# Kernel optimization log

Measured on AMD Instinct MI355X. Metric: run time of the kernel, lower is better.

## Reference

```python
import jax, jax.numpy as jnp
import numpy as np
from functools import partial

N_NODES = 50000
N_EDGES = 600000
IN_C = 128
HID = 128
OUT_C = 8
N_GRAPHS = 64
EPS = 1e-5


def setup_inputs() -> dict:
    key = jax.random.key(0)
    ks = jax.random.split(key, 16)
    inp = {
        "x": jax.random.normal(ks[0], (N_NODES, IN_C), dtype=jnp.float32),
        "edge_index": jax.random.randint(ks[1], (2, N_EDGES), 0, N_NODES, dtype=jnp.int64),
        "batch": jnp.sort(jax.random.randint(ks[2], (N_NODES,), 0, N_GRAPHS, dtype=jnp.int64)),
    }
    dims = [(IN_C, HID), (HID, HID), (HID, HID)]
    for i, (din, dout) in enumerate(dims):
        inp[f"W{i}"] = jax.random.normal(ks[3 + i], (din, dout), dtype=jnp.float32) / np.sqrt(din)
        inp[f"b{i}"] = jnp.zeros((dout,), dtype=jnp.float32)
        inp[f"g{i}"] = jnp.ones((dout,), dtype=jnp.float32)
        inp[f"be{i}"] = jnp.zeros((dout,), dtype=jnp.float32)
    inp["Wh"] = jax.random.normal(ks[10], (HID, OUT_C), dtype=jnp.float32) / np.sqrt(HID)
    inp["bh"] = jnp.zeros((OUT_C,), dtype=jnp.float32)
    return inp


def gcn_conv(x, W, b, src, dst, dinv_src, dinv_dst):
    # transform then normalized scatter-add aggregation (add_self_loops=False)
    h = x @ W  # [N, D]
    msg = (dinv_src * dinv_dst)[:, None] * h[src]  # [E, D]
    out = jax.ops.segment_sum(msg, dst, num_segments=N_NODES)
    return out + b


def batchnorm(x, g, be):
    mu = jnp.mean(x, axis=0)
    var = jnp.mean((x - mu) ** 2, axis=0)  # biased, as torch BN training
    return (x - mu) * jax.lax.rsqrt(var + EPS) * g + be


def reference(x, edge_index, batch, W0, b0, g0, be0, W1, b1, g1, be1, W2, b2, g2, be2, Wh, bh):
    src, dst = edge_index[0], edge_index[1]
    deg = jax.ops.segment_sum(jnp.ones((N_EDGES,), x.dtype), dst, num_segments=N_NODES)
    dinv = jnp.where(deg > 0, jax.lax.rsqrt(jnp.maximum(deg, 1.0)), 0.0)
    dinv_src, dinv_dst = dinv[src], dinv[dst]

    for W, b, g, be in [(W0, b0, g0, be0), (W1, b1, g1, be1), (W2, b2, g2, be2)]:
        x = gcn_conv(x, W, b, src, dst, dinv_src, dinv_dst)
        x = jax.nn.relu(batchnorm(x, g, be))  # dropout is identity in eval

    # global mean pool over graphs
    sums = jax.ops.segment_sum(x, batch, num_segments=N_GRAPHS)
    cnts = jax.ops.segment_sum(jnp.ones((N_NODES,), x.dtype), batch, num_segments=N_GRAPHS)
    pooled = sums / jnp.maximum(cnts, 1.0)[:, None]
    return pooled @ Wh + bh
```

## Files before the change

### kernel.cpp

```cpp
#include <hip/hip_runtime.h>
#include <hip/hip_fp16.h>

#define NODES 50000
#define EDGES 600000
#define C     128
#define NGRAPH 64
#define EPSBN 1e-5f
#define BUCKET 64
#define AGGNB 6250
#define POOLROWS 32
#define POOLB ((NODES + POOLROWS - 1) / POOLROWS)

typedef short v8s __attribute__((ext_vector_type(8)));
typedef float v4f __attribute__((ext_vector_type(4)));

#define OFF_DEGCNT 0u
#define OFF_CURSOR 200192u
#define OFF_STATS  400384u
#define OFF_PSUM   424960u
#define ZERO_BYTES 457728u
#define OFF_DINV   457728u
#define OFF_BPACK  657920u
#define OFF_EC     756224u
#define OFF_BUFH   13556224u
#define OFF_BUFA   26356224u

static __device__ __forceinline__ unsigned short f2bf(float f) {
    unsigned u = __float_as_uint(f);
    u += 0x7fffu + ((u >> 16) & 1u);
    return (unsigned short)(u >> 16);
}
static __device__ __forceinline__ float bflo(unsigned u) { return __uint_as_float(u << 16); }
static __device__ __forceinline__ float bfhi(unsigned u) { return __uint_as_float(u & 0xffff0000u); }
static __device__ __forceinline__ float bf1(unsigned short s) { return __uint_as_float(((unsigned)s) << 16); }

static __device__ __forceinline__ void gld_lds16(const void* g, void* l) {
    __builtin_amdgcn_global_load_lds(
        (const __attribute__((address_space(1))) void*)g,
        (__attribute__((address_space(3))) void*)l, 16, 0, 0);
}

__global__ void deg_kernel(const int* __restrict__ dst, int* __restrict__ degcnt) {
    int e4 = blockIdx.x * 256 + threadIdx.x;
    if (e4 < EDGES / 4) {
        int4 d = *(const int4*)&dst[e4 * 4];
        atomicAdd(&degcnt[d.x], 1);
        atomicAdd(&degcnt[d.y], 1);
        atomicAdd(&degcnt[d.z], 1);
        atomicAdd(&degcnt[d.w], 1);
    }
}

__global__ __launch_bounds__(256) void dinvpack_kernel(const int* __restrict__ degcnt,
                                                       float* __restrict__ dinv,
                                                       const float* __restrict__ W0,
                                                       const float* __restrict__ W1,
                                                       const float* __restrict__ W2,
                                                       short* __restrict__ Bp) {
    int bid = blockIdx.x, t = threadIdx.x;
    if (bid < 196) {
        int i = bid * 256 + t;
        if (i < NODES) {
            int v = degcnt[i];
            dinv[i] = (v > 0) ? rsqrtf((float)v) : 0.f;
        }
        return;
    }
    int id = (bid - 196) * 256 + t;
    int l = id >> 11;
    int f = id & 2047;
    const float* W = (l == 0) ? W0 : (l == 1) ? W1 : W2;
    int lane = f & 63, nbks = f >> 6;
    int nb = nbks >> 2, ks = nbks & 3;
    int q = lane >> 4, n = lane & 15;
    v8s o;
    #pragma unroll
    for (int j = 0; j < 8; j++)
        o[j] = (short)f2bf(W[(ks * 32 + q * 8 + j) * 128 + nb * 16 + n]);
    *(v8s*)&Bp[id * 8] = o;
}

__global__ void fill_kernel(const int* __restrict__ src, const int* __restrict__ dst,
                            int* __restrict__ cursor, const float* __restrict__ dinv,
                            unsigned* __restrict__ ec) {
    int e2 = blockIdx.x * 256 + threadIdx.x;
    if (e2 < EDGES / 2) {
        int2 s = *(const int2*)&src[e2 * 2];
        int2 d = *(const int2*)&dst[e2 * 2];
        float w0 = dinv[s.x] * dinv[d.x];
        float w1 = dinv[s.y] * dinv[d.y];
        unsigned r0 = (unsigned)s.x | ((unsigned)__half_as_ushort(__float2half(w0)) << 16);
        unsigned r1 = (unsigned)s.y | ((unsigned)__half_as_ushort(__float2half(w1)) << 16);
        int p0 = atomicAdd(&cursor[d.x], 1);
        if (p0 < BUCKET) ec[d.x * BUCKET + p0] = r0;
        int p1 = atomicAdd(&cursor[d.y], 1);
        if (p1 < BUCKET) ec[d.y * BUCKET + p1] = r1;
    }
}

template<bool A32>
__global__ __launch_bounds__(256) void gemm_kernel(
    const void* __restrict__ Ain, const short* __restrict__ Bpg,
    unsigned short* __restrict__ Hout, const float* __restrict__ stats,
    const float* __restrict__ g, const float* __restrict__ be) {
    __shared__ short Apk[8320];
    __shared__ short Bpk[16384];
    __shared__ float sbn[256];
    int t = threadIdx.x;
    int r0 = blockIdx.x * 64;
    if (stats) {
        if (t < 128) {
            float s = 0.f, sq = 0.f;
            #pragma unroll
            for (int r = 0; r < 8; r++) {
                s  += stats[r * 256 + t];
                sq += stats[r * 256 + 128 + t];
            }
            float mean = s * (1.0f / NODES);
            float var = sq * (1.0f / NODES) - mean * mean;
            float sc = g[t] * rsqrtf(var + EPSBN);
            sbn[t] = sc;
            sbn[128 + t] = be[t] - mean * sc;
        }
        __syncthreads();
    }
    {
        int wl = t & 63;
        int wb = t & 192;
        #pragma unroll
        for (int i = 0; i < 8; i++) {
            int cb = i * 256 + wb;
            gld_lds16(&Bpg[(size_t)(cb + wl) * 8], &Bpk[cb * 8]);
        }
    }
    #pragma unroll
    for (int i = 0; i < 4; i++) {
        int f = t + 256 * i;
        int row = f >> 4, kf = f & 15;
        int gr = r0 + row;
        float v[8];
        #pragma unroll
        for (int e = 0; e < 8; e++) v[e] = 0.f;
        if (gr < NODES) {
            if (A32) {
                const float* Ap = (const float*)Ain + (size_t)gr * C + kf * 8;
                float4 lo = *(const float4*)Ap;
                float4 hi = *(const float4*)(Ap + 4);
                v[0]=lo.x; v[1]=lo.y; v[2]=lo.z; v[3]=lo.w;
                v[4]=hi.x; v[5]=hi.y; v[6]=hi.z; v[7]=hi.w;
            } else {
                const unsigned short* Ap = (const unsigned short*)Ain + (size_t)gr * C + kf * 8;
                uint4 raw = *(const uint4*)Ap;
                v[0]=bflo(raw.x); v[1]=bfhi(raw.x); v[2]=bflo(raw.y); v[3]=bfhi(raw.y);
                v[4]=bflo(raw.z); v[5]=bfhi(raw.z); v[6]=bflo(raw.w); v[7]=bfhi(raw.w);
            }
        }
        if (stats) {
            #pragma unroll
            for (int e = 0; e < 8; e++) {
                int c = kf * 8 + e;
                v[e] = fmaxf(0.f, fmaf(v[e], sbn[c], sbn[128 + c]));
            }
        }
        v8s af;
        #pragma unroll
        for (int e = 0; e < 8; e++) af[e] = (short)f2bf(v[e]);
        int mb = row >> 4, m = row & 15, ks = kf >> 2, q = kf & 3;
        *(v8s*)&Apk[(mb * 4 + ks) * 520 + (q * 16 + m) * 8] = af;
    }
    __syncthreads();
    int lane = t & 63, mb = t >> 6;
    v4f acc[8];
    #pragma unroll
    for (int nb = 0; nb < 8; nb++) acc[nb] = 0.f;
    #pragma unroll
    for (int ks = 0; ks < 4; ks++) {
        v8s aF = *(const v8s*)&Apk[(mb * 4 + ks) * 520 + lane * 8];
        #pragma unroll
        for (int nb = 0; nb < 8; nb++) {
            v8s bF = *(const v8s*)&Bpk[((nb * 4 + ks) * 64 + lane) * 8];
            acc[nb] = __builtin_amdgcn_mfma_f32_16x16x32_bf16(aF, bF, acc[nb], 0, 0, 0);
        }
    }
    int q = lane >> 4, n = lane & 15;
    #pragma unroll
    for (int nb = 0; nb < 8; nb++) {
        #pragma unroll
        for (int r = 0; r < 4; r++)
            Apk[mb * 2080 + (q * 4 + r) * 128 + nb * 16 + n] = (short)f2bf(acc[nb][r]);
    }
    #pragma unroll
    for (int i = 0; i < 4; i++) {
        int idx = lane + 64 * i;
        int row = idx >> 4, colv = (idx & 15) * 8;
        int gr = r0 + mb * 16 + row;
        if (gr < NODES)
            *(uint4*)&Hout[(size_t)gr * C + colv] = *(const uint4*)&Apk[mb * 2080 + row * 128 + colv];
    }
}

__global__ __launch_bounds__(512) void agg_kernel(
    const unsigned short* __restrict__ H, const int* __restrict__ deg,
    const unsigned* __restrict__ ec, unsigned short* __restrict__ Aout,
    float* __restrict__ stats) {
    int t = threadIdx.x;
    int lane = t & 63;
    int half = lane >> 5;
    int sl = lane & 31;
    int wid = (blockIdx.x * 512 + t) >> 6;
    float a0 = 0.f, a1 = 0.f, a2 = 0.f, a3 = 0.f;
    unsigned o0 = 0, o1 = 0;
    if (wid < NODES) {
        int beg = wid * BUCKET;
        int end = beg + min(deg[wid], BUCKET);
        int i = beg;
        for (; i + 16 <= end; i += 16) {
            unsigned e[8];
            #pragma unroll
            for (int u = 0; u < 8; u++) e[u] = ec[i + 2 * u + half];
            uint2 v[8];
            #pragma unroll
            for (int u = 0; u < 8; u++)
                v[u] = *(const uint2*)&H[(size_t)(e[u] & 0xffffu) * C + sl * 4];
            #pragma unroll
            for (int u = 0; u < 8; u++) {
                float w = __half2float(__ushort_as_half((unsigned short)(e[u] >> 16)));
                a0 = fmaf(w, bflo(v[u].x), a0);
                a1 = fmaf(w, bfhi(v[u].x), a1);
                a2 = fmaf(w, bflo(v[u].y), a2);
                a3 = fmaf(w, bfhi(v[u].y), a3);
            }
        }
        if (i < end) {
            int last = end - 1;
            unsigned e[8];
            #pragma unroll
            for (int u = 0; u < 8; u++) {
                int idx = i + 2 * u + half;
                unsigned r = ec[idx < end ? idx : last];
                e[u] = (idx < end) ? r : (r & 0xffffu);
            }
            uint2 v[8];
            #pragma unroll
            for (int u = 0; u < 8; u++)
                v[u] = *(const uint2*)&H[(size_t)(e[u] & 0xffffu) * C + sl * 4];
            #pragma unroll
            for (int u = 0; u < 8; u++) {
                float w = __half2float(__ushort_as_half((unsigned short)(e[u] >> 16)));
                a0 = fmaf(w, bflo(v[u].x), a0);
                a1 = fmaf(w, bfhi(v[u].x), a1);
                a2 = fmaf(w, bflo(v[u].y), a2);
                a3 = fmaf(w, bfhi(v[u].y), a3);
            }
        }
        a0 += __shfl_xor(a0, 32);
        a1 += __shfl_xor(a1, 32);
        a2 += __shfl_xor(a2, 32);
        a3 += __shfl_xor(a3, 32);
        o0 = ((unsigned)f2bf(a1) << 16) | (unsigned)f2bf(a0);
        o1 = ((unsigned)f2bf(a3) << 16) | (unsigned)f2bf(a2);
        if (half == 0)
            *(uint2*)&Aout[(size_t)wid * C + sl * 4] = make_uint2(o0, o1);
    }
    __shared__ float red[2048];
    int w = t >> 6;
    {
        float r0v = bflo(o0), r1v = bfhi(o0), r2v = bflo(o1), r3v = bfhi(o1);
        float* dst = &red[1024 * half + w * 128 + sl * 4];
        if (half) { r0v *= r0v; r1v *= r1v; r2v *= r2v; r3v *= r3v; }
        dst[0] = r0v; dst[1] = r1v; dst[2] = r2v; dst[3] = r3v;
    }
    __syncthreads();
    float* sr = stats + (blockIdx.x & 7) * 256;
    if (t < 128) {
        float vs = 0.f, vq = 0.f;
        #pragma unroll
        for (int k = 0; k < 8; k++) {
            vs += red[k * 128 + t];
            vq += red[1024 + k * 128 + t];
        }
        atomicAdd(&sr[t], vs);
        atomicAdd(&sr[128 + t], vq);
    }
}

__global__ __launch_bounds__(256) void pool_kernel(const unsigned short* __restrict__ X,
                                                   const int* __restrict__ batch,
                                                   const float* __restrict__ stats,
                                                   const float* __restrict__ g,
                                                   const float* __restrict__ be,
                                                   float* __restrict__ psum) {
    int t = threadIdx.x;
    __shared__ float sbn[256];
    if (t < 128) {
        float s = 0.f, sq = 0.f;
        #pragma unroll
        for (int r = 0; r < 8; r++) {
            s  += stats[r * 256 + t];
            sq += stats[r * 256 + 128 + t];
        }
        float mean = s * (1.0f / NODES);
        float var = sq * (1.0f / NODES) - mean * mean;
        float scv = g[t] * rsqrtf(var + EPSBN);
        sbn[t] = scv;
        sbn[128 + t] = be[t] - mean * scv;
    }
    __syncthreads();
    int lane = t & 63, w = t >> 6;
    int c0 = lane * 2;
    int r0 = blockIdx.x * POOLROWS + w * 8;
    float* pr = psum + (blockIdx.x & 3) * (NGRAPH * C);
    if (r0 >= NODES) return;
    int nr = min(8, NODES - r0);
    float sc0 = sbn[c0], sh0 = sbn[128 + c0];
    float sc1 = sbn[c0 + 1], sh1 = sbn[128 + c0 + 1];
    unsigned uv[8]; int gb[8];
    #pragma unroll
    for (int j = 0; j < 8; j++) {
        int r = r0 + ((j < nr) ? j : (nr - 1));
        uv[j] = *(const unsigned*)&X[(size_t)r * C + c0];
        gb[j] = batch[r];
    }
    float ax = 0.f, ay = 0.f;
    int cur = gb[0];
    #pragma unroll
    for (int j = 0; j < 8; j++) {
        if (gb[j] != cur) {
            atomicAdd(&pr[cur * C + c0], ax);
            atomicAdd(&pr[cur * C + c0 + 1], ay);
            ax = 0.f; ay = 0.f; cur = gb[j];
        }
        float m = (j < nr) ? 1.f : 0.f;
        ax += m * fmaxf(0.f, fmaf(bflo(uv[j]), sc0, sh0));
        ay += m * fmaxf(0.f, fmaf(bfhi(uv[j]), sc1, sh1));
    }
    atomicAdd(&pr[cur * C + c0], ax);
    atomicAdd(&pr[cur * C + c0 + 1], ay);
}

__global__ __launch_bounds__(128) void head_kernel(const float* __restrict__ psum,
                                                   const int* __restrict__ batch,
                                                   const float* __restrict__ Wh,
                                                   const float* __restrict__ bh,
                                                   float* __restrict__ out) {
    int g = blockIdx.x, ch = threadIdx.x;
    __shared__ int sb[2];
    if (ch < 2) {
        int tgt = g + ch;
        int lo = 0, hi = NODES;
        while (lo < hi) { int m = (lo + hi) >> 1; if (batch[m] < tgt) lo = m + 1; else hi = m; }
        sb[ch] = lo;
    }
    float pv = 0.f;
    #pragma unroll
    for (int rep = 0; rep < 4; rep++) pv += psum[rep * (NGRAPH * C) + g * C + ch];
    __shared__ float red[128 * 8];
    #pragma unroll
    for (int o = 0; o < 8; o++) red[ch * 8 + o] = pv * Wh[ch * 8 + o];
    __syncthreads();
    for (int off = 64; off >= 1; off >>= 1) {
        if (ch < off) {
            #pragma unroll
            for (int o = 0; o < 8; o++) red[ch * 8 + o] += red[(ch + off) * 8 + o];
        }
        __syncthreads();
    }
    if (ch < 8) {
        float inv = 1.0f / fmaxf((float)(sb[1] - sb[0]), 1.0f);
        out[g * 8 + ch] = fmaf(red[ch], inv, bh[ch]);
    }
}

extern "C" void kernel_launch(void* const* d_in, const int* in_sizes, int n_in,
                              void* d_out, int out_size, void* d_ws, size_t ws_size,
                              hipStream_t stream) {
    (void)in_sizes; (void)n_in; (void)out_size; (void)ws_size;
    const float* x    = (const float*)d_in[0];
    const int*   ei   = (const int*)d_in[1];
    const int*   batch= (const int*)d_in[2];
    const float* W0   = (const float*)d_in[3];
    const float* g0   = (const float*)d_in[5];
    const float* be0  = (const float*)d_in[6];
    const float* W1   = (const float*)d_in[7];
    const float* g1   = (const float*)d_in[9];
    const float* be1  = (const float*)d_in[10];
    const float* W2   = (const float*)d_in[11];
    const float* g2   = (const float*)d_in[13];
    const float* be2  = (const float*)d_in[14];
    const float* Wh   = (const float*)d_in[15];
    const float* bh   = (const float*)d_in[16];
    float* out = (float*)d_out;

    char* ws = (char*)d_ws;
    int*   degcnt = (int*)(ws + OFF_DEGCNT);
    int*   cursor = (int*)(ws + OFF_CURSOR);
    float* stats  = (float*)(ws + OFF_STATS);
    float* psum   = (float*)(ws + OFF_PSUM);
    float* dinv   = (float*)(ws + OFF_DINV);
    short* bpack  = (short*)(ws + OFF_BPACK);
    unsigned* ec  = (unsigned*)(ws + OFF_EC);
    unsigned short* bufH = (unsigned short*)(ws + OFF_BUFH);
    unsigned short* bufA = (unsigned short*)(ws + OFF_BUFA);

    (void)hipMemsetAsync(ws, 0, ZERO_BYTES, stream);

    deg_kernel<<<(EDGES / 4 + 255) / 256, 256, 0, stream>>>(ei + EDGES, degcnt);
    dinvpack_kernel<<<196 + 24, 256, 0, stream>>>(degcnt, dinv, W0, W1, W2, bpack);
    fill_kernel<<<(EDGES / 2 + 255) / 256, 256, 0, stream>>>(ei, ei + EDGES, cursor, dinv, ec);

    const int GB = (NODES + 63) / 64;

    gemm_kernel<true><<<GB, 256, 0, stream>>>(x, bpack, bufH, nullptr, nullptr, nullptr);
    agg_kernel<<<AGGNB, 512, 0, stream>>>(bufH, degcnt, ec, bufA, stats + 0);
    gemm_kernel<false><<<GB, 256, 0, stream>>>(bufA, bpack + 16384, bufH, stats + 0, g0, be0);
    agg_kernel<<<AGGNB, 512, 0, stream>>>(bufH, degcnt, ec, bufA, stats + 2048);
    gemm_kernel<false><<<GB, 256, 0, stream>>>(bufA, bpack + 32768, bufH, stats + 2048, g1, be1);
    agg_kernel<<<AGGNB, 512, 0, stream>>>(bufH, degcnt, ec, bufA, stats + 4096);
    pool_kernel<<<POOLB, 256, 0, stream>>>(bufA, batch, stats + 4096, g2, be2, psum);
    head_kernel<<<NGRAPH, 128, 0, stream>>>(psum, batch, Wh, bh, out);
}
```

Measured before the change: 302.8 us.

## Merge degree count into fill, store 16-bit edge sources, split aggregation by channel halves

Removes the separate degree kernel by reusing the fill cursor as the degree count. Edge buckets now store only the 16-bit source index, and the normalization weight is recomputed in the aggregation kernel from dinv. Each aggregation block now covers one half of the channels, so the 64-channel halves of a node are processed by different blocks and block order is interleaved to share cache. This halves the edge-list footprint and drops one preprocessing pass. In exchange it adds a dinv gather per edge, doubles the edge-list reads across channel halves, and relies on node ids fitting in 16 bits.

Measured after the change: 304.9 us. No clear change (+0.7%).

```diff
diff --git a/kernel.cpp b/kernel.cpp
--- a/kernel.cpp
+++ b/kernel.cpp
@@ -7,23 +7,22 @@
 #define NGRAPH 64
 #define EPSBN 1e-5f
 #define BUCKET 64
-#define AGGNB 6250
+#define AGGNB 12504
 #define POOLROWS 32
 #define POOLB ((NODES + POOLROWS - 1) / POOLROWS)
 
 typedef short v8s __attribute__((ext_vector_type(8)));
 typedef float v4f __attribute__((ext_vector_type(4)));
 
-#define OFF_DEGCNT 0u
-#define OFF_CURSOR 200192u
-#define OFF_STATS  400384u
-#define OFF_PSUM   424960u
-#define ZERO_BYTES 457728u
-#define OFF_DINV   457728u
-#define OFF_BPACK  657920u
-#define OFF_EC     756224u
-#define OFF_BUFH   13556224u
-#define OFF_BUFA   26356224u
+#define OFF_CURSOR 0u
+#define OFF_STATS  200192u
+#define OFF_PSUM   224768u
+#define ZERO_BYTES 257536u
+#define OFF_DINV   257536u
+#define OFF_BPACK  457728u
+#define OFF_EC     556032u
+#define OFF_BUFH   6956032u
+#define OFF_BUFA   19756032u
 
 static __device__ __forceinline__ unsigned short f2bf(float f) {
     unsigned u = __float_as_uint(f);
@@ -40,14 +39,16 @@
         (__attribute__((address_space(3))) void*)l, 16, 0, 0);
 }
 
-__global__ void deg_kernel(const int* __restrict__ dst, int* __restrict__ degcnt) {
-    int e4 = blockIdx.x * 256 + threadIdx.x;
-    if (e4 < EDGES / 4) {
-        int4 d = *(const int4*)&dst[e4 * 4];
-        atomicAdd(&degcnt[d.x], 1);
-        atomicAdd(&degcnt[d.y], 1);
-        atomicAdd(&degcnt[d.z], 1);
-        atomicAdd(&degcnt[d.w], 1);
+__global__ void fill_kernel(const int* __restrict__ src, const int* __restrict__ dst,
+                            int* __restrict__ cursor, unsigned short* __restrict__ ec16) {
+    int e2 = blockIdx.x * 256 + threadIdx.x;
+    if (e2 < EDGES / 2) {
+        int2 s = *(const int2*)&src[e2 * 2];
+        int2 d = *(const int2*)&dst[e2 * 2];
+        int p0 = atomicAdd(&cursor[d.x], 1);
+        if (p0 < BUCKET) ec16[d.x * BUCKET + p0] = (unsigned short)s.x;
+        int p1 = atomicAdd(&cursor[d.y], 1);
+        if (p1 < BUCKET) ec16[d.y * BUCKET + p1] = (unsigned short)s.y;
     }
 }
 
@@ -78,24 +79,6 @@
     for (int j = 0; j < 8; j++)
         o[j] = (short)f2bf(W[(ks * 32 + q * 8 + j) * 128 + nb * 16 + n]);
     *(v8s*)&Bp[id * 8] = o;
-}
-
-__global__ void fill_kernel(const int* __restrict__ src, const int* __restrict__ dst,
-                            int* __restrict__ cursor, const float* __restrict__ dinv,
-                            unsigned* __restrict__ ec) {
-    int e2 = blockIdx.x * 256 + threadIdx.x;
-    if (e2 < EDGES / 2) {
-        int2 s = *(const int2*)&src[e2 * 2];
-        int2 d = *(const int2*)&dst[e2 * 2];
-        float w0 = dinv[s.x] * dinv[d.x];
-        float w1 = dinv[s.y] * dinv[d.y];
-        unsigned r0 = (unsigned)s.x | ((unsigned)__half_as_ushort(__float2half(w0)) << 16);
-        unsigned r1 = (unsigned)s.y | ((unsigned)__half_as_ushort(__float2half(w1)) << 16);
-        int p0 = atomicAdd(&cursor[d.x], 1);
-        if (p0 < BUCKET) ec[d.x * BUCKET + p0] = r0;
-        int p1 = atomicAdd(&cursor[d.y], 1);
-        if (p1 < BUCKET) ec[d.y * BUCKET + p1] = r1;
-    }
 }
 
 template<bool A32>
@@ -201,86 +184,96 @@
 
 __global__ __launch_bounds__(512) void agg_kernel(
     const unsigned short* __restrict__ H, const int* __restrict__ deg,
-    const unsigned* __restrict__ ec, unsigned short* __restrict__ Aout,
-    float* __restrict__ stats) {
+    const float* __restrict__ dinv, const unsigned short* __restrict__ ec16,
+    unsigned short* __restrict__ Aout, float* __restrict__ stats) {
     int t = threadIdx.x;
     int lane = t & 63;
     int half = lane >> 5;
     int sl = lane & 31;
-    int wid = (blockIdx.x * 512 + t) >> 6;
-    float a0 = 0.f, a1 = 0.f, a2 = 0.f, a3 = 0.f;
-    unsigned o0 = 0, o1 = 0;
+    int b = blockIdx.x;
+    int xs = b & 7;
+    int h = xs >> 2;
+    int o = (b >> 3) * 4 + (xs & 3);
+    int w = t >> 6;
+    int wid = o * 8 + w;
+    int h64 = h * 64;
+    float a0 = 0.f, a1 = 0.f;
+    unsigned o0 = 0;
     if (wid < NODES) {
-        int beg = wid * BUCKET;
-        int end = beg + min(deg[wid], BUCKET);
+        int dg = min(deg[wid], BUCKET);
+        float dd = dinv[wid];
+        int beg = wid * BUCKET, end = beg + dg;
+        const unsigned short* Hc = H + h64 + sl * 2;
         int i = beg;
         for (; i + 16 <= end; i += 16) {
-            unsigned e[8];
-            #pragma unroll
-            for (int u = 0; u < 8; u++) e[u] = ec[i + 2 * u + half];
-            uint2 v[8];
-            #pragma unroll
-            for (int u = 0; u < 8; u++)
-                v[u] = *(const uint2*)&H[(size_t)(e[u] & 0xffffu) * C + sl * 4];
+            uint4 ra = *(const uint4*)&ec16[i];
+            uint4 rb = *(const uint4*)&ec16[i + 8];
+            unsigned wd[8] = {ra.x, ra.y, ra.z, ra.w, rb.x, rb.y, rb.z, rb.w};
+            int rec[8];
+            #pragma unroll
+            for (int u = 0; u < 8; u++) rec[u] = (wd[u] >> (16 * half)) & 0xffff;
+            float dv[8];
+            #pragma unroll
+            for (int u = 0; u < 8; u++) dv[u] = dinv[rec[u]];
+            unsigned v[8];
+            #pragma unroll
+            for (int u = 0; u < 8; u++) v[u] = *(const unsigned*)&Hc[(size_t)rec[u] * C];
             #pragma unroll
             for (int u = 0; u < 8; u++) {
-                float w = __half2float(__ushort_as_half((unsigned short)(e[u] >> 16)));
-                a0 = fmaf(w, bflo(v[u].x), a0);
-                a1 = fmaf(w, bfhi(v[u].x), a1);
-                a2 = fmaf(w, bflo(v[u].y), a2);
-                a3 = fmaf(w, bfhi(v[u].y), a3);
+                float wt = dv[u] * dd;
+                a0 = fmaf(wt, bflo(v[u]), a0);
+                a1 = fmaf(wt, bfhi(v[u]), a1);
             }
         }
         if (i < end) {
-            int last = end - 1;
-            unsigned e[8];
+            int rl = ec16[end - 1];
+            uint4 ra = *(const uint4*)&ec16[i];
+            uint4 rb = *(const uint4*)&ec16[i + 8];
+            unsigned wd[8] = {ra.x, ra.y, ra.z, ra.w, rb.x, rb.y, rb.z, rb.w};
+            int rec[8]; float ms[8];
             #pragma unroll
             for (int u = 0; u < 8; u++) {
                 int idx = i + 2 * u + half;
-                unsigned r = ec[idx < end ? idx : last];
-                e[u] = (idx < end) ? r : (r & 0xffffu);
-            }
-            uint2 v[8];
-            #pragma unroll
-            for (int u = 0; u < 8; u++)
-                v[u] = *(const uint2*)&H[(size_t)(e[u] & 0xffffu) * C + sl * 4];
+                int r = (wd[u] >> (16 * half)) & 0xffff;
+                bool valid = idx < end;
+                rec[u] = valid ? r : rl;
+                ms[u] = valid ? 1.f : 0.f;
+            }
+            float dv[8];
+            #pragma unroll
+            for (int u = 0; u < 8; u++) dv[u] = dinv[rec[u]];
+            unsigned v[8];
+            #pragma unroll
+            for (int u = 0; u < 8; u++) v[u] = *(const unsigned*)&Hc[(size_t)rec[u] * C];
             #pragma unroll
             for (int u = 0; u < 8; u++) {
-                float w = __half2float(__ushort_as_half((unsigned short)(e[u] >> 16)));
-                a0 = fmaf(w, bflo(v[u].x), a0);
-                a1 = fmaf(w, bfhi(v[u].x), a1);
-                a2 = fmaf(w, bflo(v[u].y), a2);
-                a3 = fmaf(w, bfhi(v[u].y), a3);
+                float wt = ms[u] * dv[u] * dd;
+                a0 = fmaf(wt, bflo(v[u]), a0);
+                a1 = fmaf(wt, bfhi(v[u]), a1);
             }
         }
         a0 += __shfl_xor(a0, 32);
         a1 += __shfl_xor(a1, 32);
-        a2 += __shfl_xor(a2, 32);
-        a3 += __shfl_xor(a3, 32);
         o0 = ((unsigned)f2bf(a1) << 16) | (unsigned)f2bf(a0);
-        o1 = ((unsigned)f2bf(a3) << 16) | (unsigned)f2bf(a2);
         if (half == 0)
-            *(uint2*)&Aout[(size_t)wid * C + sl * 4] = make_uint2(o0, o1);
-    }
-    __shared__ float red[2048];
-    int w = t >> 6;
+            *(unsigned*)&Aout[(size_t)wid * C + h64 + sl * 2] = o0;
+    }
+    __shared__ float red[1024];
     {
-        float r0v = bflo(o0), r1v = bfhi(o0), r2v = bflo(o1), r3v = bfhi(o1);
-        float* dst = &red[1024 * half + w * 128 + sl * 4];
-        if (half) { r0v *= r0v; r1v *= r1v; r2v *= r2v; r3v *= r3v; }
-        dst[0] = r0v; dst[1] = r1v; dst[2] = r2v; dst[3] = r3v;
+        float rx = bflo(o0), ry = bfhi(o0);
+        if (half) { rx *= rx; ry *= ry; }
+        red[half * 512 + w * 64 + sl * 2]     = rx;
+        red[half * 512 + w * 64 + sl * 2 + 1] = ry;
     }
     __syncthreads();
-    float* sr = stats + (blockIdx.x & 7) * 256;
+    float* sr = stats + ((b >> 3) & 7) * 256;
     if (t < 128) {
-        float vs = 0.f, vq = 0.f;
-        #pragma unroll
-        for (int k = 0; k < 8; k++) {
-            vs += red[k * 128 + t];
-            vq += red[1024 + k * 128 + t];
-        }
-        atomicAdd(&sr[t], vs);
-        atomicAdd(&sr[128 + t], vq);
+        int role = t >> 6;
+        int c = t & 63;
+        float vv = 0.f;
+        #pragma unroll
+        for (int k = 0; k < 8; k++) vv += red[role * 512 + k * 64 + c];
+        atomicAdd(&sr[role * 128 + h64 + c], vv);
     }
 }
 
@@ -392,30 +385,28 @@
     float* out = (float*)d_out;
 
     char* ws = (char*)d_ws;
-    int*   degcnt = (int*)(ws + OFF_DEGCNT);
     int*   cursor = (int*)(ws + OFF_CURSOR);
     float* stats  = (float*)(ws + OFF_STATS);
     float* psum   = (float*)(ws + OFF_PSUM);
     float* dinv   = (float*)(ws + OFF_DINV);
     short* bpack  = (short*)(ws + OFF_BPACK);
-    unsigned* ec  = (unsigned*)(ws + OFF_EC);
+    unsigned short* ec16 = (unsigned short*)(ws + OFF_EC);
     unsigned short* bufH = (unsigned short*)(ws + OFF_BUFH);
     unsigned short* bufA = (unsigned short*)(ws + OFF_BUFA);
 
     (void)hipMemsetAsync(ws, 0, ZERO_BYTES, stream);
 
-    deg_kernel<<<(EDGES / 4 + 255) / 256, 256, 0, stream>>>(ei + EDGES, degcnt);
-    dinvpack_kernel<<<196 + 24, 256, 0, stream>>>(degcnt, dinv, W0, W1, W2, bpack);
-    fill_kernel<<<(EDGES / 2 + 255) / 256, 256, 0, stream>>>(ei, ei + EDGES, cursor, dinv, ec);
+    fill_kernel<<<(EDGES / 2 + 255) / 256, 256, 0, stream>>>(ei, ei + EDGES, cursor, ec16);
+    dinvpack_kernel<<<196 + 24, 256, 0, stream>>>(cursor, dinv, W0, W1, W2, bpack);
 
     const int GB = (NODES + 63) / 64;
 
     gemm_kernel<true><<<GB, 256, 0, stream>>>(x, bpack, bufH, nullptr, nullptr, nullptr);
-    agg_kernel<<<AGGNB, 512, 0, stream>>>(bufH, degcnt, ec, bufA, stats + 0);
+    agg_kernel<<<AGGNB, 512, 0, stream>>>(bufH, cursor, dinv, ec16, bufA, stats + 0);
     gemm_kernel<false><<<GB, 256, 0, stream>>>(bufA, bpack + 16384, bufH, stats + 0, g0, be0);
-    agg_kernel<<<AGGNB, 512, 0, stream>>>(bufH, degcnt, ec, bufA, stats + 2048);
+    agg_kernel<<<AGGNB, 512, 0, stream>>>(bufH, cursor, dinv, ec16, bufA, stats + 2048);
     gemm_kernel<false><<<GB, 256, 0, stream>>>(bufA, bpack + 32768, bufH, stats + 2048, g1, be1);
-    agg_kernel<<<AGGNB, 512, 0, stream>>>(bufH, degcnt, ec, bufA, stats + 4096);
+    agg_kernel<<<AGGNB, 512, 0, stream>>>(bufH, cursor, dinv, ec16, bufA, stats + 4096);
     pool_kernel<<<POOLB, 256, 0, stream>>>(bufA, batch, stats + 4096, g2, be2, psum);
     head_kernel<<<NGRAPH, 128, 0, stream>>>(psum, batch, Wh, bh, out);
 }
```
